# Performance work log

Hardware: AMD Instinct MI355X
Metric: run time of the kernel (lower is better)

## Reference

```python
import jax, jax.numpy as jnp
import numpy as np

B, S, D, H = 2, 2048, 2048, 16
DEPTH = D // H


def setup_inputs() -> dict:
    key = jax.random.key(0)
    ks = jax.random.split(key, 12)
    std = 1.0 / np.sqrt(D)
    mk = lambda k, shape: (jax.random.uniform(k, shape, jnp.float32) * 2 - 1) * std
    # causal additive mask: 1.0 where future position (masked), 0.0 elsewhere
    mask = jnp.triu(jnp.ones((S, S), jnp.float32), k=1)[None, None]
    return {
        "q": jax.random.normal(ks[0], (B, S, D), jnp.float32),
        "k": jax.random.normal(ks[1], (B, S, D), jnp.float32),
        "v": jax.random.normal(ks[2], (B, S, D), jnp.float32),
        "mask": mask,
        "wq_w": mk(ks[3], (D, D)), "wq_b": mk(ks[4], (D,)),
        "wk_w": mk(ks[5], (D, D)), "wk_b": mk(ks[6], (D,)),
        "wv_w": mk(ks[7], (D, D)), "wv_b": mk(ks[8], (D,)),
        "dense_w": mk(ks[9], (D, D)), "dense_b": mk(ks[10], (D,)),
    }


def split_heads(x):
    # [B,S,D] -> [B,H,S,depth]
    b, s, _ = x.shape
    return x.reshape(b, s, H, DEPTH).transpose(0, 2, 1, 3)


def reference(q, k, v, mask, wq_w, wq_b, wk_w, wk_b, wv_w, wv_b, dense_w, dense_b):
    # torch Linear: y = x @ W.T + b
    qh = split_heads(q @ wq_w.T + wq_b)
    kh = split_heads(k @ wk_w.T + wk_b)
    vh = split_heads(v @ wv_w.T + wv_b)
    scale = 1.0 / jnp.sqrt(jnp.asarray(DEPTH, jnp.float32))
    logits = jnp.einsum("bhqd,bhkd->bhqk", qh, kh) * scale
    logits = logits + mask * (-1e9)
    weights = jax.nn.softmax(logits, axis=-1)  # dropout is identity in eval
    out = jnp.einsum("bhqk,bhkd->bhqd", weights, vh)
    out = out.transpose(0, 2, 1, 3).reshape(q.shape[0], -1, D)
    return out @ dense_w.T + dense_b
```

## Files before the change

kernel.cpp:

```cpp
#include <hip/hip_runtime.h>
#include <hip/hip_bf16.h>


typedef __bf16 bf16x8 __attribute__((ext_vector_type(8)));
typedef float f32x4 __attribute__((ext_vector_type(4)));
typedef float f32x16 __attribute__((ext_vector_type(16)));
typedef unsigned short u16;
typedef unsigned int u32;

#define DEV static __device__ __forceinline__

DEV void gload_lds16(const void* g, void* l) {
  __builtin_amdgcn_global_load_lds(
      (const __attribute__((address_space(1))) void*)g,
      (__attribute__((address_space(3))) void*)l, 16, 0, 0);
}

DEV f32x4 mfma16(bf16x8 a, bf16x8 b, f32x4 c) {
  return __builtin_amdgcn_mfma_f32_16x16x32_bf16(a, b, c, 0, 0, 0);
}

DEV f32x16 mfma32(bf16x8 a, bf16x8 b, f32x16 c) {
  return __builtin_amdgcn_mfma_f32_32x32x16_bf16(a, b, c, 0, 0, 0);
}

DEV u16 f2bf(float x) {
  return __builtin_bit_cast(u16, __float2bfloat16(x));
}

DEV u32 pack2(float lo, float hi_) {
  return (u32)f2bf(lo) | ((u32)f2bf(hi_) << 16);
}

#define BAR() __builtin_amdgcn_s_barrier()

__global__ void __launch_bounds__(256) conv_f32_bf16(
    const float* __restrict__ in, u16* __restrict__ out) {
  const size_t i = ((size_t)blockIdx.x * 256 + threadIdx.x) * 4;
  const float4 v = *reinterpret_cast<const float4*>(in + i);
  ushort4 o;
  o.x = f2bf(v.x); o.y = f2bf(v.y); o.z = f2bf(v.z); o.w = f2bf(v.w);
  *reinterpret_cast<ushort4*>(out + i) = o;
}

__global__ void __launch_bounds__(256) conv_all(
    const float* __restrict__ s0, const float* __restrict__ s1,
    const float* __restrict__ s2, const float* __restrict__ s3,
    const float* __restrict__ s4, const float* __restrict__ s5,
    const float* __restrict__ s6,
    u16* __restrict__ d0, u16* __restrict__ d1, u16* __restrict__ d2,
    u16* __restrict__ d3, u16* __restrict__ d4, u16* __restrict__ d5,
    u16* __restrict__ d6, const size_t nact, const size_t nw) {
  const int j = blockIdx.y;
  const size_t i = ((size_t)blockIdx.x * 256 + threadIdx.x) * 4;
  const float* s; u16* d; size_t n;
  switch (j) {
    case 0: s = s0; d = d0; n = nact; break;
    case 1: s = s1; d = d1; n = nact; break;
    case 2: s = s2; d = d2; n = nact; break;
    case 3: s = s3; d = d3; n = nw; break;
    case 4: s = s4; d = d4; n = nw; break;
    case 5: s = s5; d = d5; n = nw; break;
    default: s = s6; d = d6; n = nw; break;
  }
  if (i >= n) return;
  const float4 v = *reinterpret_cast<const float4*>(s + i);
  ushort4 o;
  o.x = f2bf(v.x); o.y = f2bf(v.y); o.z = f2bf(v.z); o.w = f2bf(v.w);
  *reinterpret_cast<ushort4*>(d + i) = o;
}

#define GK 2048

DEV void gemm128_core(const u16* __restrict__ A, const u16* __restrict__ Bw,
                      const float* __restrict__ bias, void* __restrict__ Cout,
                      const int m0, const int n0, const int N,
                      const int out_f32, u16* AsB, u16* BsB) {
  const int tid = threadIdx.x;
  const int lane = tid & 63;
  const int wid = tid >> 6;
  const int wr = wid >> 1, wc = wid & 1;
  const int g = lane >> 4;
  const int r16 = lane & 15;

  int offA[2], offB[2], dstE[2];
#pragma unroll
  for (int rr = 0; rr < 2; ++rr) {
    const int G = rr * 256 + tid;
    const int rp = G >> 3;
    const int s = (G & 7) ^ (rp & 7);
    const int row = rp * 2 + (s >> 2);
    const int ch = s & 3;
    offA[rr] = (m0 + row) * GK + ch * 8;
    offB[rr] = (n0 + row) * GK + ch * 8;
    dstE[rr] = rr * 2048 + wid * 512;
  }

#define STAGE_A(kt, kh) do {                                              \
    u16* base_ = AsB + (((kt) & 1) * 2 + (kh)) * 4096;                    \
    const int go_ = (kt) * 64 + (kh) * 32;                                \
    gload_lds16(A + (size_t)(offA[0] + go_), base_ + dstE[0]);            \
    gload_lds16(A + (size_t)(offA[1] + go_), base_ + dstE[1]);            \
  } while (0)
#define STAGE_B(kt, kh) do {                                              \
    u16* base_ = BsB + (((kt) & 1) * 2 + (kh)) * 4096;                    \
    const int go_ = (kt) * 64 + (kh) * 32;                                \
    gload_lds16(Bw + (size_t)(offB[0] + go_), base_ + dstE[0]);           \
    gload_lds16(Bw + (size_t)(offB[1] + go_), base_ + dstE[1]);           \
  } while (0)
#define READ_A(MH, buf) do {                                              \
    _Pragma("unroll") for (int i_ = 0; i_ < 2; ++i_) {                    \
      const int row_ = wr * 64 + ((MH) * 2 + i_) * 16 + r16;              \
      const int rp_ = row_ >> 1;                                          \
      const int sl_ = (((row_ & 1) << 2) | g) ^ (rp_ & 7);                \
      const int off_ = rp_ * 64 + sl_ * 8;                                \
      af[i_][0] = *(const bf16x8*)(AsB + ((buf) * 2 + 0) * 4096 + off_);  \
      af[i_][1] = *(const bf16x8*)(AsB + ((buf) * 2 + 1) * 4096 + off_);  \
    } } while (0)
#define READ_B(NH, buf, bf) do {                                          \
    _Pragma("unroll") for (int j_ = 0; j_ < 2; ++j_) {                    \
      const int row_ = wc * 64 + ((NH) * 2 + j_) * 16 + r16;              \
      const int rp_ = row_ >> 1;                                          \
      const int sl_ = (((row_ & 1) << 2) | g) ^ (rp_ & 7);                \
      const int off_ = rp_ * 64 + sl_ * 8;                                \
      bf[j_][0] = *(const bf16x8*)(BsB + ((buf) * 2 + 0) * 4096 + off_);  \
      bf[j_][1] = *(const bf16x8*)(BsB + ((buf) * 2 + 1) * 4096 + off_);  \
    } } while (0)
#define MFMA_Q(MH, NH, bf) do {                                           \
    __builtin_amdgcn_s_setprio(1);                                        \
    _Pragma("unroll") for (int i_ = 0; i_ < 2; ++i_)                      \
    _Pragma("unroll") for (int j_ = 0; j_ < 2; ++j_) {                    \
      f32x4 c_ = acc[(MH) * 2 + i_][(NH) * 2 + j_];                       \
      c_ = mfma16(af[i_][0], bf[j_][0], c_);                              \
      c_ = mfma16(af[i_][1], bf[j_][1], c_);                              \
      acc[(MH) * 2 + i_][(NH) * 2 + j_] = c_;                             \
    }                                                                     \
    __builtin_amdgcn_s_setprio(0);                                        \
  } while (0)

  f32x4 acc[4][4];
#pragma unroll
  for (int i = 0; i < 4; ++i)
#pragma unroll
    for (int j = 0; j < 4; ++j) acc[i][j] = {0.f, 0.f, 0.f, 0.f};

  bf16x8 af[2][2], bf0[2][2], bf1[2][2];

  STAGE_B(0, 0); STAGE_B(0, 1); STAGE_A(0, 0); STAGE_A(0, 1);
  STAGE_B(1, 0); STAGE_B(1, 1);
  asm volatile("s_waitcnt vmcnt(4)" ::: "memory");
  BAR();

  for (int it = 0; it < 16; ++it) {
    const bool tail = (it == 15);
    const int t0 = 2 * it, t1 = t0 + 1;
    READ_A(0, 0); READ_B(0, 0, bf0);
    STAGE_A(t1, 0);
    BAR(); MFMA_Q(0, 0, bf0); BAR();
    READ_B(1, 0, bf1);
    STAGE_A(t1, 1);
    BAR(); MFMA_Q(0, 1, bf1); BAR();
    READ_A(1, 0);
    if (!tail) STAGE_B(t0 + 2, 0);
    BAR(); MFMA_Q(1, 0, bf0); BAR();
    if (!tail) STAGE_B(t0 + 2, 1);
    BAR(); MFMA_Q(1, 1, bf1); BAR();
    READ_A(0, 1); READ_B(0, 1, bf0);
    if (!tail) {
      STAGE_A(t0 + 2, 0);
      asm volatile("s_waitcnt vmcnt(6)" ::: "memory");
    } else {
      asm volatile("s_waitcnt vmcnt(0)" ::: "memory");
    }
    BAR(); MFMA_Q(0, 0, bf0); BAR();
    READ_B(1, 1, bf1);
    if (!tail) STAGE_A(t0 + 2, 1);
    BAR(); MFMA_Q(0, 1, bf1); BAR();
    READ_A(1, 1);
    if (!tail) STAGE_B(t1 + 2, 0);
    BAR(); MFMA_Q(1, 0, bf0); BAR();
    if (!tail) {
      STAGE_B(t1 + 2, 1);
      asm volatile("s_waitcnt vmcnt(4)" ::: "memory");
    } else {
      asm volatile("s_waitcnt vmcnt(0)" ::: "memory");
    }
    BAR(); MFMA_Q(1, 1, bf1); BAR();
  }

  const int rbase = m0 + wr * 64 + g * 4;
  const int cb = n0 + wc * 64 + r16;
#pragma unroll
  for (int i = 0; i < 4; ++i) {
#pragma unroll
    for (int j = 0; j < 4; ++j) {
      const int c = cb + j * 16;
      const float bv = bias[c];
#pragma unroll
      for (int r = 0; r < 4; ++r) {
        const float v = acc[i][j][r] + bv;
        const size_t idx = (size_t)(rbase + i * 16 + r) * N + c;
        if (out_f32) ((float*)Cout)[idx] = v;
        else ((u16*)Cout)[idx] = f2bf(v);
      }
    }
  }
#undef STAGE_A
#undef STAGE_B
#undef READ_A
#undef READ_B
#undef MFMA_Q
}

__global__ void __launch_bounds__(256, 2) gemm_qkv3(
    const u16* __restrict__ A0, const u16* __restrict__ A1,
    const u16* __restrict__ A2, const u16* __restrict__ W0,
    const u16* __restrict__ W1, const u16* __restrict__ W2,
    const float* __restrict__ b0, const float* __restrict__ b1,
    const float* __restrict__ b2, u16* __restrict__ C0,
    u16* __restrict__ C1, u16* __restrict__ C2) {
  __shared__ u16 AsB[4 * 4096];
  __shared__ u16 BsB[4 * 4096];
  const int logical = (blockIdx.x & 7) * 192 + (blockIdx.x >> 3);
  const int which = logical >> 9;
  const int inner = logical & 511;
  const int m0 = (inner & 31) << 7;
  const int n0 = (inner >> 5) << 7;
  const u16* A = which == 0 ? A0 : which == 1 ? A1 : A2;
  const u16* W = which == 0 ? W0 : which == 1 ? W1 : W2;
  const float* bb = which == 0 ? b0 : which == 1 ? b1 : b2;
  u16* C = which == 0 ? C0 : which == 1 ? C1 : C2;
  gemm128_core(A, W, bb, C, m0, n0, 2048, 0, AsB, BsB);
}

__global__ void __launch_bounds__(256, 2) gemm_one(
    const u16* __restrict__ A, const u16* __restrict__ Bw,
    const float* __restrict__ bias, void* __restrict__ Cout,
    const int out_f32) {
  __shared__ u16 AsB[4 * 4096];
  __shared__ u16 BsB[4 * 4096];
  const int logical = (blockIdx.x & 7) * 64 + (blockIdx.x >> 3);
  const int m0 = (logical & 31) << 7;
  const int n0 = (logical >> 5) << 7;
  gemm128_core(A, Bw, bias, Cout, m0, n0, 2048, out_f32, AsB, BsB);
}

#define SEQ 2048
#define DMODEL 2048
#define DH 128
#define QBLK 128
#define KBLK 64
#define C1 0.12751744f
#define THR_RAW 62.73f

__global__ void __launch_bounds__(256, 2) flash_attn(
    const u16* __restrict__ Qh, const u16* __restrict__ Kh,
    const u16* __restrict__ Vh, u16* __restrict__ O) {
  __shared__ u16 Ks[2][KBLK * DH];
  __shared__ u16 Vt[DH * KBLK];

  const int tid = threadIdx.x;
  const int lane = tid & 63;
  const int w = tid >> 6;
  const int hi = lane >> 5;
  const int l31 = lane & 31;

  const int cc = blockIdx.x;
  const int low = cc & 15;
  const int bh = (cc >> 4) & 31;
  const int h = bh & 15;
  const int b = bh >> 4;
  const int g0 = low ^ h;
  const int qt = b ? (15 - g0) : g0;
  const int q0 = qt * QBLK;
  const size_t rowbase = (size_t)b * SEQ;
  const int hoff = h * DH;
  const int qw = q0 + w * 32;
  const int qlane = qw + l31;

  bf16x8 aq[8];
  {
    const u16* qp = &Qh[(rowbase + qlane) * DMODEL + hoff + hi * 8];
#pragma unroll
    for (int c = 0; c < 8; ++c)
      aq[c] = *reinterpret_cast<const bf16x8*>(qp + c * 16);
  }

  f32x16 oacc[4];
#pragma unroll
  for (int dt = 0; dt < 4; ++dt)
#pragma unroll
    for (int r = 0; r < 16; ++r) oacc[dt][r] = 0.f;
  float mrow = -1e30f, lrow = 0.f;

  const int krl = w * 16 + (lane >> 4);
  const int kg4 = w * 4 + (lane >> 4);
  const int du = lane & 15;

  const int nkt = 2 * qt + 2;
  const int ktd = qw >> 6;

  auto stageK = [&](int kt) {
#pragma unroll
    for (int i = 0; i < 4; ++i) {
      const int r = krl + i * 4;
      const int cg = (lane & 15) ^ (r & 15);
      gload_lds16(&Kh[(rowbase + kt * KBLK + r) * DMODEL + hoff + cg * 8],
                  &Ks[kt & 1][(w * 16 + i * 4) * DH]);
    }
  };

  stageK(0);
  uint4 vv[4];
#pragma unroll
  for (int r = 0; r < 4; ++r)
    vv[r] = *reinterpret_cast<const uint4*>(
        &Vh[(rowbase + kg4 * 4 + r) * DMODEL + hoff + du * 8]);

  for (int kt = 0; kt < nkt; ++kt) {
    const int k0 = kt * KBLK;
    if (kt + 1 < nkt) {
      stageK(kt + 1);
      asm volatile("s_waitcnt vmcnt(4)" ::: "memory");
    } else {
      asm volatile("s_waitcnt vmcnt(0)" ::: "memory");
    }

#pragma unroll
    for (int j = 0; j < 8; ++j) {
      const int d = du * 8 + j;
      ushort4 pk4;
      pk4.x = ((const u16*)&vv[0])[j];
      pk4.y = ((const u16*)&vv[1])[j];
      pk4.z = ((const u16*)&vv[2])[j];
      pk4.w = ((const u16*)&vv[3])[j];
      const int slot = (((kg4 >> 1) ^ ((d >> 2) & 7)) * 8) + (kg4 & 1) * 4;
      *reinterpret_cast<ushort4*>(&Vt[d * KBLK + slot]) = pk4;
    }
    asm volatile("s_waitcnt lgkmcnt(0)" ::: "memory");
    BAR();

    const bool active = (kt <= ktd);
    const u16* kb = &Ks[kt & 1][0];
    float p[2][16];
    bool act1 = false;

    if (active) {
      const bool diag = (kt == ktd);
      act1 = (kt < ktd) || (w & 1);
      const bool m0q = diag && !(w & 1);
      const bool m1q = diag && (w & 1);
      {
        f32x16 s;
#pragma unroll
        for (int r = 0; r < 16; ++r) s[r] = 0.f;
        __builtin_amdgcn_s_setprio(1);
#pragma unroll
        for (int c = 0; c < 8; ++c) {
          const int row = l31;
          const bf16x8 kf = *reinterpret_cast<const bf16x8*>(
              &kb[row * DH + (((c * 2 + hi) ^ (row & 15)) * 8)]);
          s = mfma32(kf, aq[c], s);
        }
        __builtin_amdgcn_s_setprio(0);
#pragma unroll
        for (int r = 0; r < 16; ++r) {
          const int krow = (r & 3) + 8 * (r >> 2) + 4 * hi;
          p[0][r] = (m0q && (k0 + krow > qlane)) ? -1e9f : s[r];
        }
      }
      if (act1) {
        f32x16 s;
#pragma unroll
        for (int r = 0; r < 16; ++r) s[r] = 0.f;
        __builtin_amdgcn_s_setprio(1);
#pragma unroll
        for (int c = 0; c < 8; ++c) {
          const int row = 32 + l31;
          const bf16x8 kf = *reinterpret_cast<const bf16x8*>(
              &kb[row * DH + (((c * 2 + hi) ^ (row & 15)) * 8)]);
          s = mfma32(kf, aq[c], s);
        }
        __builtin_amdgcn_s_setprio(0);
#pragma unroll
        for (int r = 0; r < 16; ++r) {
          const int krow = (r & 3) + 8 * (r >> 2) + 4 * hi;
          p[1][r] = (m1q && (k0 + 32 + krow > qlane)) ? -1e9f : s[r];
        }
      } else {
#pragma unroll
        for (int r = 0; r < 16; ++r) p[1][r] = -1e9f;
      }
    }

    if (kt + 1 < nkt) {
#pragma unroll
      for (int r = 0; r < 4; ++r)
        vv[r] = *reinterpret_cast<const uint4*>(
            &Vh[(rowbase + k0 + KBLK + kg4 * 4 + r) * DMODEL + hoff + du * 8]);
    }

    if (active) {
      float mx = fmaxf(p[0][0], p[0][1]);
#pragma unroll
      for (int r = 2; r < 16; ++r) mx = fmaxf(mx, p[0][r]);
#pragma unroll
      for (int r = 0; r < 16; ++r) mx = fmaxf(mx, p[1][r]);
      mx = fmaxf(mx, __shfl_xor(mx, 32));

      const bool need = (mx > mrow + THR_RAW);
      if (__any((int)need)) {
        const float mn = fmaxf(mrow, mx);
        const float al = exp2f((mrow - mn) * C1);
        mrow = mn;
        lrow *= al;
#pragma unroll
        for (int r = 0; r < 16; ++r) {
          const float ar = __shfl(al, (r & 3) + 8 * (r >> 2) + 4 * hi);
#pragma unroll
          for (int dt = 0; dt < 4; ++dt) oacc[dt][r] *= ar;
        }
      }

      float sum = 0.f;
#pragma unroll
      for (int t = 0; t < 2; ++t)
#pragma unroll
        for (int r = 0; r < 16; ++r) {
          p[t][r] = exp2f((p[t][r] - mrow) * C1);
          sum += p[t][r];
        }
      sum += __shfl_xor(sum, 32);
      lrow += sum;

      u32 pk[2][8];
#pragma unroll
      for (int t = 0; t < 2; ++t)
#pragma unroll
        for (int m = 0; m < 8; ++m)
          pk[t][m] = pack2(p[t][2 * m], p[t][2 * m + 1]);

      __builtin_amdgcn_s_setprio(1);
#pragma unroll
      for (int ks = 0; ks < 4; ++ks) {
        if (ks >= 2 && !act1) break;
        const int t = ks >> 1;
        const int bs = (ks & 1) * 4;
        const u32 s0 = __shfl_xor(pk[t][bs + 0], 32);
        const u32 s1 = __shfl_xor(pk[t][bs + 1], 32);
        const u32 s2 = __shfl_xor(pk[t][bs + 2], 32);
        const u32 s3 = __shfl_xor(pk[t][bs + 3], 32);
        union { u32 u[4]; bf16x8 v; } pa;
        pa.u[0] = hi ? s2 : pk[t][bs + 0];
        pa.u[1] = hi ? s3 : pk[t][bs + 1];
        pa.u[2] = hi ? pk[t][bs + 2] : s0;
        pa.u[3] = hi ? pk[t][bs + 3] : s1;
#pragma unroll
        for (int dt = 0; dt < 4; ++dt) {
          const int d = dt * 32 + l31;
          const bf16x8 vf = *reinterpret_cast<const bf16x8*>(
              &Vt[d * KBLK + (((ks * 2 + hi) ^ ((d >> 2) & 7)) * 8)]);
          oacc[dt] = mfma32(pa.v, vf, oacc[dt]);
        }
      }
      __builtin_amdgcn_s_setprio(0);
    }

    BAR();
  }

  const float li = __builtin_amdgcn_rcpf(lrow);
#pragma unroll
  for (int r = 0; r < 16; ++r) {
    const int rowq = (r & 3) + 8 * (r >> 2) + 4 * hi;
    const float lr = __shfl(li, rowq);
    u16* op = &O[(rowbase + qw + rowq) * DMODEL + hoff + l31];
#pragma unroll
    for (int dt = 0; dt < 4; ++dt) op[dt * 32] = f2bf(oacc[dt][r] * lr);
  }
}

extern "C" void kernel_launch(void* const* d_in, const int* in_sizes, int n_in,
                              void* d_out, int out_size, void* d_ws,
                              size_t ws_size, hipStream_t stream) {
  const int Bv = 2, S = 2048, D = 2048;
  const int M = Bv * S;
  const size_t NT = (size_t)M * D;
  const size_t NW = (size_t)D * D;

  const float* q = (const float*)d_in[0];
  const float* k = (const float*)d_in[1];
  const float* v = (const float*)d_in[2];
  const float* wq_w = (const float*)d_in[4];
  const float* wq_b = (const float*)d_in[5];
  const float* wk_w = (const float*)d_in[6];
  const float* wk_b = (const float*)d_in[7];
  const float* wv_w = (const float*)d_in[8];
  const float* wv_b = (const float*)d_in[9];
  const float* dw = (const float*)d_in[10];
  const float* db = (const float*)d_in[11];
  float* out = (float*)d_out;

  const dim3 blk(256);
  const dim3 gattn(512);
  const size_t need = (7 * NT + 4 * NW) * 2;

  if (ws_size >= need) {
    u16* base = (u16*)d_ws;
    u16* Xq = base;
    u16* Xk = Xq + NT;
    u16* Xv = Xk + NT;
    u16* Wq = Xv + NT;
    u16* Wk = Wq + NW;
    u16* Wv = Wk + NW;
    u16* Wd = Wv + NW;
    u16* Qh = Wd + NW;
    u16* Kh = Qh + NT;
    u16* Vh = Kh + NT;
    u16* Obf = Vh + NT;

    conv_all<<<dim3((unsigned)(NT / 1024), 7), blk, 0, stream>>>(
        q, k, v, wq_w, wk_w, wv_w, dw, Xq, Xk, Xv, Wq, Wk, Wv, Wd, NT, NW);
    gemm_qkv3<<<dim3(1536), blk, 0, stream>>>(
        Xq, Xk, Xv, Wq, Wk, Wv, wq_b, wk_b, wv_b, Qh, Kh, Vh);
    flash_attn<<<gattn, blk, 0, stream>>>(Qh, Kh, Vh, Obf);
    gemm_one<<<dim3(512), blk, 0, stream>>>(Obf, Wd, db, out, 1);
  } else {
    u16* Xbf = (u16*)d_ws;
    u16* Wbf = Xbf + NT;
    u16* Qh = Wbf + NW;
    u16* Kh = Qh + NT;
    u16* Vh = Kh + NT;
    u16* Obf = Vh + NT;
    const dim3 gact((unsigned)(NT / 1024));
    const dim3 gw((unsigned)(NW / 1024));

    conv_f32_bf16<<<gact, blk, 0, stream>>>(q, Xbf);
    conv_f32_bf16<<<gw, blk, 0, stream>>>(wq_w, Wbf);
    gemm_one<<<dim3(512), blk, 0, stream>>>(Xbf, Wbf, wq_b, Qh, 0);
    conv_f32_bf16<<<gact, blk, 0, stream>>>(k, Xbf);
    conv_f32_bf16<<<gw, blk, 0, stream>>>(wk_w, Wbf);
    gemm_one<<<dim3(512), blk, 0, stream>>>(Xbf, Wbf, wk_b, Kh, 0);
    conv_f32_bf16<<<gact, blk, 0, stream>>>(v, Xbf);
    conv_f32_bf16<<<gw, blk, 0, stream>>>(wv_w, Wbf);
    gemm_one<<<dim3(512), blk, 0, stream>>>(Xbf, Wbf, wv_b, Vh, 0);
    flash_attn<<<gattn, blk, 0, stream>>>(Qh, Kh, Vh, Obf);
    conv_f32_bf16<<<gw, blk, 0, stream>>>(dw, Wbf);
    gemm_one<<<dim3(512), blk, 0, stream>>>(Obf, Wbf, db, out, 1);
  }
}
```

Baseline: 322.5 us.

## Remap GEMM tiles per XCD, move vmcnt wait earlier, split softmax reductions

The GEMM block-to-tile mapping now gives each XCD a contiguous band of M rows, so tiles sharing A rows land on the same L2. The GEMM main loop moves one vmcnt wait to an earlier phase, which may change how load latency overlaps with MFMA work. The attention softmax max and sum reductions are split into four independent accumulators to shorten the dependency chains. The earlier wait can stall the pipeline sooner, and the changed summation order slightly alters the floating-point results.

```diff
diff --git a/kernel.cpp b/kernel.cpp
--- a/kernel.cpp
+++ b/kernel.cpp
@@ -163,15 +163,15 @@
     READ_A(1, 0);
     if (!tail) STAGE_B(t0 + 2, 0);
     BAR(); MFMA_Q(1, 0, bf0); BAR();
-    if (!tail) STAGE_B(t0 + 2, 1);
+    if (!tail) {
+      STAGE_B(t0 + 2, 1);
+      asm volatile("s_waitcnt vmcnt(4)" ::: "memory");
+    } else {
+      asm volatile("s_waitcnt vmcnt(0)" ::: "memory");
+    }
     BAR(); MFMA_Q(1, 1, bf1); BAR();
     READ_A(0, 1); READ_B(0, 1, bf0);
-    if (!tail) {
-      STAGE_A(t0 + 2, 0);
-      asm volatile("s_waitcnt vmcnt(6)" ::: "memory");
-    } else {
-      asm volatile("s_waitcnt vmcnt(0)" ::: "memory");
-    }
+    if (!tail) STAGE_A(t0 + 2, 0);
     BAR(); MFMA_Q(0, 0, bf0); BAR();
     READ_B(1, 1, bf1);
     if (!tail) STAGE_A(t0 + 2, 1);
@@ -221,11 +221,12 @@
     u16* __restrict__ C1, u16* __restrict__ C2) {
   __shared__ u16 AsB[4 * 4096];
   __shared__ u16 BsB[4 * 4096];
-  const int logical = (blockIdx.x & 7) * 192 + (blockIdx.x >> 3);
-  const int which = logical >> 9;
-  const int inner = logical & 511;
-  const int m0 = (inner & 31) << 7;
-  const int n0 = (inner >> 5) << 7;
+  const int xcd = blockIdx.x & 7;
+  const int t = blockIdx.x >> 3;
+  const int which = t >> 6;
+  const int r = t & 63;
+  const int m0 = (xcd * 4 + (r >> 4)) << 7;
+  const int n0 = (r & 15) << 7;
   const u16* A = which == 0 ? A0 : which == 1 ? A1 : A2;
   const u16* W = which == 0 ? W0 : which == 1 ? W1 : W2;
   const float* bb = which == 0 ? b0 : which == 1 ? b1 : b2;
@@ -239,9 +240,10 @@
     const int out_f32) {
   __shared__ u16 AsB[4 * 4096];
   __shared__ u16 BsB[4 * 4096];
-  const int logical = (blockIdx.x & 7) * 64 + (blockIdx.x >> 3);
-  const int m0 = (logical & 31) << 7;
-  const int n0 = (logical >> 5) << 7;
+  const int xcd = blockIdx.x & 7;
+  const int t = blockIdx.x >> 3;
+  const int m0 = (xcd * 4 + (t >> 4)) << 7;
+  const int n0 = (t & 15) << 7;
   gemm128_core(A, Bw, bias, Cout, m0, n0, 2048, out_f32, AsB, BsB);
 }
 
@@ -401,11 +403,18 @@
     }
 
     if (active) {
-      float mx = fmaxf(p[0][0], p[0][1]);
-#pragma unroll
-      for (int r = 2; r < 16; ++r) mx = fmaxf(mx, p[0][r]);
-#pragma unroll
-      for (int r = 0; r < 16; ++r) mx = fmaxf(mx, p[1][r]);
+      float mx0 = fmaxf(p[0][0], p[1][0]);
+      float mx1 = fmaxf(p[0][1], p[1][1]);
+      float mx2 = fmaxf(p[0][2], p[1][2]);
+      float mx3 = fmaxf(p[0][3], p[1][3]);
+#pragma unroll
+      for (int r = 4; r < 16; r += 4) {
+        mx0 = fmaxf(mx0, fmaxf(p[0][r + 0], p[1][r + 0]));
+        mx1 = fmaxf(mx1, fmaxf(p[0][r + 1], p[1][r + 1]));
+        mx2 = fmaxf(mx2, fmaxf(p[0][r + 2], p[1][r + 2]));
+        mx3 = fmaxf(mx3, fmaxf(p[0][r + 3], p[1][r + 3]));
+      }
+      float mx = fmaxf(fmaxf(mx0, mx1), fmaxf(mx2, mx3));
       mx = fmaxf(mx, __shfl_xor(mx, 32));
 
       const bool need = (mx > mrow + THR_RAW);
@@ -422,14 +431,19 @@
         }
       }
 
-      float sum = 0.f;
+      float s0 = 0.f, s1 = 0.f, s2 = 0.f, s3 = 0.f;
 #pragma unroll
       for (int t = 0; t < 2; ++t)
 #pragma unroll
-        for (int r = 0; r < 16; ++r) {
-          p[t][r] = exp2f((p[t][r] - mrow) * C1);
-          sum += p[t][r];
-        }
+        for (int r = 0; r < 16; r += 4) {
+          p[t][r + 0] = exp2f((p[t][r + 0] - mrow) * C1);
+          p[t][r + 1] = exp2f((p[t][r + 1] - mrow) * C1);
+          p[t][r + 2] = exp2f((p[t][r + 2] - mrow) * C1);
+          p[t][r + 3] = exp2f((p[t][r + 3] - mrow) * C1);
+          s0 += p[t][r + 0]; s1 += p[t][r + 1];
+          s2 += p[t][r + 2]; s3 += p[t][r + 3];
+        }
+      float sum = (s0 + s1) + (s2 + s3);
       sum += __shfl_xor(sum, 32);
       lrow += sum;
 
@@ -446,15 +460,15 @@
         if (ks >= 2 && !act1) break;
         const int t = ks >> 1;
         const int bs = (ks & 1) * 4;
-        const u32 s0 = __shfl_xor(pk[t][bs + 0], 32);
-        const u32 s1 = __shfl_xor(pk[t][bs + 1], 32);
-        const u32 s2 = __shfl_xor(pk[t][bs + 2], 32);
-        const u32 s3 = __shfl_xor(pk[t][bs + 3], 32);
+        const u32 q0s = __shfl_xor(pk[t][bs + 0], 32);
+        const u32 q1s = __shfl_xor(pk[t][bs + 1], 32);
+        const u32 q2s = __shfl_xor(pk[t][bs + 2], 32);
+        const u32 q3s = __shfl_xor(pk[t][bs + 3], 32);
         union { u32 u[4]; bf16x8 v; } pa;
-        pa.u[0] = hi ? s2 : pk[t][bs + 0];
-        pa.u[1] = hi ? s3 : pk[t][bs + 1];
-        pa.u[2] = hi ? pk[t][bs + 2] : s0;
-        pa.u[3] = hi ? pk[t][bs + 3] : s1;
+        pa.u[0] = hi ? q2s : pk[t][bs + 0];
+        pa.u[1] = hi ? q3s : pk[t][bs + 1];
+        pa.u[2] = hi ? pk[t][bs + 2] : q0s;
+        pa.u[3] = hi ? pk[t][bs + 3] : q1s;
 #pragma unroll
         for (int dt = 0; dt < 4; ++dt) {
           const int d = dt * 32 + l31;
```

Measured after the change: 298.3 us. 7.5% less time.
